# Kernel optimization log

Hardware: AMD Instinct MI355X
Metric: run time of the kernel (lower is better)

Reference implementation:

```python
import jax, jax.numpy as jnp
import numpy as np

HIDDEN = 1536
BOTTLENECK = 128
LN_EPS = 1e-5


def setup_inputs() -> dict:
    key = jax.random.key(0)
    k1, k2, k3 = jax.random.split(key, 3)
    hidden_states = jax.random.normal(k1, (4, 4096, HIDDEN), dtype=jnp.float32)
    # xavier_uniform with gain=0.01: bound = gain * sqrt(6/(fan_in+fan_out))
    bound = 0.01 * np.sqrt(6.0 / (HIDDEN + BOTTLENECK))
    w_down = jax.random.uniform(k2, (BOTTLENECK, HIDDEN), minval=-bound, maxval=bound, dtype=jnp.float32)
    w_up = jax.random.uniform(k3, (HIDDEN, BOTTLENECK), minval=-bound, maxval=bound, dtype=jnp.float32)
    ln_gamma = jnp.ones((HIDDEN,), dtype=jnp.float32)
    ln_beta = jnp.zeros((HIDDEN,), dtype=jnp.float32)
    return {"hidden_states": hidden_states, "w_down": w_down, "w_up": w_up,
            "ln_gamma": ln_gamma, "ln_beta": ln_beta}


def _fourier_2d(x):
    # fp32 FFT round-trip along seq (axis=1) then feature (axis=2), ortho norm
    orig_dtype = x.dtype
    xf = x.astype(jnp.float32)
    f = jnp.fft.fft(xf, axis=1, norm='ortho')
    f = jnp.fft.fft(f, axis=2, norm='ortho')
    t = jnp.fft.ifft(f, axis=2, norm='ortho')
    t = jnp.fft.ifft(t, axis=1, norm='ortho')
    return jnp.real(t).astype(orig_dtype)


def reference(hidden_states, w_down, w_up, ln_gamma, ln_beta):
    residual = hidden_states
    # down_proj: [b,s,H] @ [H,B] -> [b,s,B]   (nn.Linear uses x @ W^T)
    x = jnp.einsum('bsh,dh->bsd', hidden_states, w_down)
    # dropout is identity in eval mode
    x = _fourier_2d(x)
    # up_proj: [b,s,B] -> [b,s,H]
    x = jnp.einsum('bsd,hd->bsh', x, w_up)
    y = residual + x
    mu = jnp.mean(y, axis=-1, keepdims=True)
    var = jnp.mean(jnp.square(y - mu), axis=-1, keepdims=True)
    return (y - mu) * jax.lax.rsqrt(var + LN_EPS) * ln_gamma + ln_beta
```

## Files before the change

### kernel.cpp

```cpp
#include <hip/hip_runtime.h>

#define H 1536
#define BD 128
#define ROWS 16
#define NTHREADS 512
#define NBLOCKS 1024

using f16x8 = _Float16 __attribute__((ext_vector_type(8)));
using f16x4 = _Float16 __attribute__((ext_vector_type(4)));
using f32x4 = float __attribute__((ext_vector_type(4)));
using i64x2 = long __attribute__((ext_vector_type(2)));

#define WD_SCALE 16384.0f
#define T8_SCALE (1.0f/128.0f)
#define X_SCALE  (1.0f/2097152.0f)

__global__ __launch_bounds__(256) void pack_weights(const float* __restrict__ wd,
                                                    const float* __restrict__ wu,
                                                    char* __restrict__ wdp8,
                                                    char* __restrict__ wup8) {
    int f = blockIdx.x * 256 + threadIdx.x;
    const float* src;
    char* dst;
    if (f < 24576) {
        int w = f / 3072, rem = f - w * 3072;
        int ph = rem >> 6, l = rem & 63;
        int row = 16 * w + (l & 15);
        int col = 32 * ph + 8 * (l >> 4);
        src = wd + (size_t)row * H + col;
        int p = ph >> 1, half = ph & 1;
        dst = wdp8 + (((size_t)(w * 24 + p) * 64 + l) * 16 + half * 8);
    } else {
        int g = f - 24576;
        int w = g / 3072, rem = g - w * 3072;
        int t2 = rem >> 6, l = rem & 63;
        int nf = t2 >> 2, kf = t2 & 3;
        int row = 192 * w + 16 * nf + (l & 15);
        int col = 32 * kf + 8 * (l >> 4);
        src = wu + (size_t)row * BD + col;
        int q = nf * 2 + (kf >> 1), half = kf & 1;
        dst = wup8 + (((size_t)(w * 24 + q) * 64 + l) * 16 + half * 8);
    }
    float4 v0 = reinterpret_cast<const float4*>(src)[0];
    float4 v1 = reinterpret_cast<const float4*>(src)[1];
    int i0 = __builtin_amdgcn_cvt_pk_fp8_f32(v0.x * WD_SCALE, v0.y * WD_SCALE, 0, false);
    i0     = __builtin_amdgcn_cvt_pk_fp8_f32(v0.z * WD_SCALE, v0.w * WD_SCALE, i0, true);
    int i1 = __builtin_amdgcn_cvt_pk_fp8_f32(v1.x * WD_SCALE, v1.y * WD_SCALE, 0, false);
    i1     = __builtin_amdgcn_cvt_pk_fp8_f32(v1.z * WD_SCALE, v1.w * WD_SCALE, i1, true);
    int2 st = {i0, i1};
    *reinterpret_cast<int2*>(dst) = st;
}

__global__ __launch_bounds__(NTHREADS, 4) void fused_adapter(
    const float* __restrict__ hs,
    const char* __restrict__ wdp8,
    const char* __restrict__ wup8,
    const float* __restrict__ gamma,
    const float* __restrict__ beta,
    float* __restrict__ out)
{
    __shared__ alignas(16) char smem[76800];
    _Float16* hsb = reinterpret_cast<_Float16*>(smem);
    char* hsa8    = smem + 49152;
    char* tb8     = smem + 73728;
    float* redS   = reinterpret_cast<float*>(smem + 75776);
    float* redQ   = redS + 128;

    const int tid  = threadIdx.x;
    const int lane = tid & 63;
    const int w    = tid >> 6;
    const int l15  = lane & 15;
    const int lk   = lane >> 4;
    const long row0 = (long)blockIdx.x * ROWS;
    const float* hsblk = hs + row0 * H;

    const i64x2* wp2 = reinterpret_cast<const i64x2*>(wdp8) + (size_t)w * 24 * 64 + lane;
    const i64x2* up2 = reinterpret_cast<const i64x2*>(wup8) + (size_t)w * 24 * 64 + lane;

    const int sr  = tid >> 5;
    const int scg = tid & 31;
    const int swzs = (sr & 7) << 3;
    const float* srow = hsblk + (long)sr * H + scg * 8;

    auto store_chunk = [&](int c, float4 va, float4 vb) {
        int col8 = 8 * scg + 256 * c;
        f16x8 hv;
        hv[0] = (_Float16)va.x; hv[1] = (_Float16)va.y;
        hv[2] = (_Float16)va.z; hv[3] = (_Float16)va.w;
        hv[4] = (_Float16)vb.x; hv[5] = (_Float16)vb.y;
        hv[6] = (_Float16)vb.z; hv[7] = (_Float16)vb.w;
        *reinterpret_cast<f16x8*>(&hsb[sr * H + (col8 ^ swzs)]) = hv;
        int c8 = scg + 32 * c;
        int kk = c8 >> 2, m = c8 & 3;
        int al = (16 * m + sr) ^ ((kk & 15) << 1);
        int j0 = __builtin_amdgcn_cvt_pk_fp8_f32(va.x, va.y, 0, false);
        j0     = __builtin_amdgcn_cvt_pk_fp8_f32(va.z, va.w, j0, true);
        int j1 = __builtin_amdgcn_cvt_pk_fp8_f32(vb.x, vb.y, 0, false);
        j1     = __builtin_amdgcn_cvt_pk_fp8_f32(vb.z, vb.w, j1, true);
        int2 stv = {j0, j1};
        *reinterpret_cast<int2*>(&hsa8[(kk * 64 + al) * 8]) = stv;
    };

    i64x2 bq[4];
#pragma unroll
    for (int i = 0; i < 4; ++i) bq[i] = wp2[i * 64];

    float4 A0, B0, A1, B1;
    A0 = reinterpret_cast<const float4*>(srow)[0];
    B0 = reinterpret_cast<const float4*>(srow)[1];
    A1 = reinterpret_cast<const float4*>(srow + 256)[0];
    B1 = reinterpret_cast<const float4*>(srow + 256)[1];
    store_chunk(0, A0, B0);
    store_chunk(1, A1, B1);
    __syncthreads();

    f32x4 accv[4] = {{0,0,0,0},{0,0,0,0},{0,0,0,0},{0,0,0,0}};
#pragma unroll
    for (int g = 0; g < 3; ++g) {
        if (g < 2) {
            const float4* p0 = reinterpret_cast<const float4*>(srow + 256 * (2 * g + 2));
            const float4* p1 = reinterpret_cast<const float4*>(srow + 256 * (2 * g + 3));
            A0 = p0[0]; B0 = p0[1];
            A1 = p1[0]; B1 = p1[1];
        }
#pragma unroll
        for (int i = 0; i < 8; ++i) {
            int p = 8 * g + i;
            int kk0 = 2 * p, kk1 = 2 * p + 1;
            long blo = *reinterpret_cast<const long*>(&hsa8[(kk0 * 64 + (lane ^ ((kk0 & 15) << 1))) * 8]);
            long bhi = *reinterpret_cast<const long*>(&hsa8[(kk1 * 64 + (lane ^ ((kk1 & 15) << 1))) * 8]);
            i64x2 b = bq[p & 3];
            if (p + 4 < 24) bq[p & 3] = wp2[(p + 4) * 64];
            f32x4 a = accv[p & 3];
            a = __builtin_amdgcn_mfma_f32_16x16x32_fp8_fp8(b[0], blo, a, 0, 0, 0);
            a = __builtin_amdgcn_mfma_f32_16x16x32_fp8_fp8(b[1], bhi, a, 0, 0, 0);
            accv[p & 3] = a;
        }
        if (g < 2) {
            store_chunk(2 * g + 2, A0, B0);
            store_chunk(2 * g + 3, A1, B1);
            __syncthreads();
        }
    }

    i64x2 uq[4];
#pragma unroll
    for (int i = 0; i < 4; ++i) uq[i] = up2[i * 64];

    {
        f32x4 t0 = (accv[0] + accv[1]) + (accv[2] + accv[3]);
        int p0 = __builtin_amdgcn_cvt_pk_fp8_f32(t0[0] * T8_SCALE, t0[1] * T8_SCALE, 0, false);
        int p1 = __builtin_amdgcn_cvt_pk_fp8_f32(t0[2] * T8_SCALE, t0[3] * T8_SCALE, 0, false);
        unsigned word = (unsigned)(p0 & 0xFFFF) | ((unsigned)(p1 & 0xFFFF) << 16);
        int c0 = 16 * w + 4 * lk;
        int kf = c0 >> 5, hi = (c0 >> 3) & 3, off = c0 & 7;
        *reinterpret_cast<unsigned*>(&tb8[(kf * 64 + hi * 16 + l15) * 8 + off]) = word;
    }
    __syncthreads();

    long a2f8[4];
#pragma unroll
    for (int kf = 0; kf < 4; ++kf)
        a2f8[kf] = *reinterpret_cast<const long*>(&tb8[(kf * 64 + lane) * 8]);

    float s = 0.f, q = 0.f;
#pragma unroll
    for (int nf = 0; nf < 12; ++nf) {
        i64x2 u0 = uq[(2 * nf) & 3];
        i64x2 u1 = uq[(2 * nf + 1) & 3];
        if (2 * nf + 4 < 24) uq[(2 * nf) & 3]     = up2[(2 * nf + 4) * 64];
        if (2 * nf + 5 < 24) uq[(2 * nf + 1) & 3] = up2[(2 * nf + 5) * 64];
        f32x4 acc = {0.f, 0.f, 0.f, 0.f};
        acc = __builtin_amdgcn_mfma_f32_16x16x32_fp8_fp8(u0[0], a2f8[0], acc, 0, 0, 0);
        acc = __builtin_amdgcn_mfma_f32_16x16x32_fp8_fp8(u0[1], a2f8[1], acc, 0, 0, 0);
        acc = __builtin_amdgcn_mfma_f32_16x16x32_fp8_fp8(u1[0], a2f8[2], acc, 0, 0, 0);
        acc = __builtin_amdgcn_mfma_f32_16x16x32_fp8_fp8(u1[1], a2f8[3], acc, 0, 0, 0);
        int cx = 192 * w + 16 * nf + 4 * lk;
        int idx = l15 * H + (cx ^ ((l15 & 7) << 3));
        f16x4 hv4 = *reinterpret_cast<const f16x4*>(&hsb[idx]);
        float y0 = acc[0] * X_SCALE + (float)hv4[0];
        float y1 = acc[1] * X_SCALE + (float)hv4[1];
        float y2 = acc[2] * X_SCALE + (float)hv4[2];
        float y3 = acc[3] * X_SCALE + (float)hv4[3];
        s += (y0 + y1) + (y2 + y3);
        q += (y0 * y0 + y1 * y1) + (y2 * y2 + y3 * y3);
        f16x4 yv;
        yv[0] = (_Float16)y0; yv[1] = (_Float16)y1;
        yv[2] = (_Float16)y2; yv[3] = (_Float16)y3;
        *reinterpret_cast<f16x4*>(&hsb[idx]) = yv;
    }

    s += __shfl_xor(s, 16); s += __shfl_xor(s, 32);
    q += __shfl_xor(q, 16); q += __shfl_xor(q, 32);
    if (lane < 16) {
        redS[w * 16 + lane] = s;
        redQ[w * 16 + lane] = q;
    }
    __syncthreads();

    {
        const int fr  = tid >> 5;
        const int cid = tid & 31;
        const int fswz = (fr & 7) << 3;
        float S = 0.f, Q = 0.f;
#pragma unroll
        for (int ww = 0; ww < 8; ++ww) {
            S += redS[ww * 16 + fr];
            Q += redQ[ww * 16 + fr];
        }
        float mean = S * (1.0f / (float)H);
        float var  = Q * (1.0f / (float)H) - mean * mean;
        float rstd = rsqrtf(var + 1e-5f);
        float* orow = out + (row0 + fr) * H;
#pragma unroll
        for (int k = 0; k < 6; ++k) {
            int col = 8 * (cid + 32 * k);
            f16x8 yv = *reinterpret_cast<const f16x8*>(&hsb[fr * H + (col ^ fswz)]);
            const float4* gp = reinterpret_cast<const float4*>(gamma + col);
            const float4* bp = reinterpret_cast<const float4*>(beta + col);
            float4 g0 = gp[0], g1 = gp[1];
            float4 b0 = bp[0], b1 = bp[1];
            float4 o0, o1;
            o0.x = ((float)yv[0] - mean) * rstd * g0.x + b0.x;
            o0.y = ((float)yv[1] - mean) * rstd * g0.y + b0.y;
            o0.z = ((float)yv[2] - mean) * rstd * g0.z + b0.z;
            o0.w = ((float)yv[3] - mean) * rstd * g0.w + b0.w;
            o1.x = ((float)yv[4] - mean) * rstd * g1.x + b1.x;
            o1.y = ((float)yv[5] - mean) * rstd * g1.y + b1.y;
            o1.z = ((float)yv[6] - mean) * rstd * g1.z + b1.z;
            o1.w = ((float)yv[7] - mean) * rstd * g1.w + b1.w;
            float4* op = reinterpret_cast<float4*>(orow + col);
            op[0] = o0;
            op[1] = o1;
        }
    }
}

extern "C" void kernel_launch(void* const* d_in, const int* in_sizes, int n_in,
                              void* d_out, int out_size, void* d_ws, size_t ws_size,
                              hipStream_t stream) {
    const float* hs    = (const float*)d_in[0];
    const float* wd    = (const float*)d_in[1];
    const float* wu    = (const float*)d_in[2];
    const float* gam   = (const float*)d_in[3];
    const float* bet   = (const float*)d_in[4];
    float* out = (float*)d_out;

    char* wdp8 = (char*)d_ws;
    char* wup8 = (char*)d_ws + (size_t)128 * H;

    pack_weights<<<192, 256, 0, stream>>>(wd, wu, wdp8, wup8);
    fused_adapter<<<NBLOCKS, NTHREADS, 0, stream>>>(hs, wdp8, wup8, gam, bet, out);
}
```

Before: 56.25 us.

## Make blocks process four row tiles with double-buffered LDS prefetch

Each block now handles four 16-row tiles instead of one, and the grid shrinks to 256 blocks. The LDS staging buffers are double-buffered so the next tile's hidden states are loaded, converted and stored in chunks interleaved with the current tile's down-projection, up-projection and LayerNorm phases. The aim is to hide global-load latency behind compute and to avoid the per-block prologue. In exchange, LDS use roughly doubles to about 150 KB per block, which allows only one block per CU. Each thread also keeps only one chunk of loads in flight, so memory-level parallelism may drop.

```diff
diff --git a/kernel.cpp b/kernel.cpp
--- a/kernel.cpp
+++ b/kernel.cpp
@@ -4,7 +4,7 @@
 #define BD 128
 #define ROWS 16
 #define NTHREADS 512
-#define NBLOCKS 1024
+#define NBLOCKS 256
 
 using f16x8 = _Float16 __attribute__((ext_vector_type(8)));
 using f16x4 = _Float16 __attribute__((ext_vector_type(4)));
@@ -51,7 +51,7 @@
     *reinterpret_cast<int2*>(dst) = st;
 }
 
-__global__ __launch_bounds__(NTHREADS, 4) void fused_adapter(
+__global__ __launch_bounds__(NTHREADS, 2) void fused_adapter(
     const float* __restrict__ hs,
     const char* __restrict__ wdp8,
     const char* __restrict__ wup8,
@@ -59,20 +59,21 @@
     const float* __restrict__ beta,
     float* __restrict__ out)
 {
-    __shared__ alignas(16) char smem[76800];
-    _Float16* hsb = reinterpret_cast<_Float16*>(smem);
-    char* hsa8    = smem + 49152;
-    char* tb8     = smem + 73728;
-    float* redS   = reinterpret_cast<float*>(smem + 75776);
-    float* redQ   = redS + 128;
+    __shared__ alignas(16) char smem[150528];
+    _Float16* hsbP = reinterpret_cast<_Float16*>(smem);
+    char*     hsa8P = smem + 49152;
+    _Float16* hsbQ = reinterpret_cast<_Float16*>(smem + 73728);
+    char*     hsa8Q = smem + 122880;
+    char*     tb8   = smem + 147456;
+    float*    redS  = reinterpret_cast<float*>(smem + 149504);
+    float*    redQ  = redS + 128;
 
     const int tid  = threadIdx.x;
     const int lane = tid & 63;
     const int w    = tid >> 6;
     const int l15  = lane & 15;
     const int lk   = lane >> 4;
-    const long row0 = (long)blockIdx.x * ROWS;
-    const float* hsblk = hs + row0 * H;
+    const long row0 = (long)blockIdx.x * (4 * ROWS);
 
     const i64x2* wp2 = reinterpret_cast<const i64x2*>(wdp8) + (size_t)w * 24 * 64 + lane;
     const i64x2* up2 = reinterpret_cast<const i64x2*>(wup8) + (size_t)w * 24 * 64 + lane;
@@ -80,16 +81,15 @@
     const int sr  = tid >> 5;
     const int scg = tid & 31;
     const int swzs = (sr & 7) << 3;
-    const float* srow = hsblk + (long)sr * H + scg * 8;
-
-    auto store_chunk = [&](int c, float4 va, float4 vb) {
+
+    auto store_chunk = [&](_Float16* hsb_, char* hsa8_, int c, float4 va, float4 vb) {
         int col8 = 8 * scg + 256 * c;
         f16x8 hv;
         hv[0] = (_Float16)va.x; hv[1] = (_Float16)va.y;
         hv[2] = (_Float16)va.z; hv[3] = (_Float16)va.w;
         hv[4] = (_Float16)vb.x; hv[5] = (_Float16)vb.y;
         hv[6] = (_Float16)vb.z; hv[7] = (_Float16)vb.w;
-        *reinterpret_cast<f16x8*>(&hsb[sr * H + (col8 ^ swzs)]) = hv;
+        *reinterpret_cast<f16x8*>(&hsb_[sr * H + (col8 ^ swzs)]) = hv;
         int c8 = scg + 32 * c;
         int kk = c8 >> 2, m = c8 & 3;
         int al = (16 * m + sr) ^ ((kk & 15) << 1);
@@ -98,141 +98,173 @@
         int j1 = __builtin_amdgcn_cvt_pk_fp8_f32(vb.x, vb.y, 0, false);
         j1     = __builtin_amdgcn_cvt_pk_fp8_f32(vb.z, vb.w, j1, true);
         int2 stv = {j0, j1};
-        *reinterpret_cast<int2*>(&hsa8[(kk * 64 + al) * 8]) = stv;
+        *reinterpret_cast<int2*>(&hsa8_[(kk * 64 + al) * 8]) = stv;
     };
 
-    i64x2 bq[4];
-#pragma unroll
-    for (int i = 0; i < 4; ++i) bq[i] = wp2[i * 64];
-
-    float4 A0, B0, A1, B1;
-    A0 = reinterpret_cast<const float4*>(srow)[0];
-    B0 = reinterpret_cast<const float4*>(srow)[1];
-    A1 = reinterpret_cast<const float4*>(srow + 256)[0];
-    B1 = reinterpret_cast<const float4*>(srow + 256)[1];
-    store_chunk(0, A0, B0);
-    store_chunk(1, A1, B1);
-    __syncthreads();
-
-    f32x4 accv[4] = {{0,0,0,0},{0,0,0,0},{0,0,0,0},{0,0,0,0}};
-#pragma unroll
-    for (int g = 0; g < 3; ++g) {
-        if (g < 2) {
-            const float4* p0 = reinterpret_cast<const float4*>(srow + 256 * (2 * g + 2));
-            const float4* p1 = reinterpret_cast<const float4*>(srow + 256 * (2 * g + 3));
-            A0 = p0[0]; B0 = p0[1];
-            A1 = p1[0]; B1 = p1[1];
-        }
-#pragma unroll
-        for (int i = 0; i < 8; ++i) {
-            int p = 8 * g + i;
-            int kk0 = 2 * p, kk1 = 2 * p + 1;
-            long blo = *reinterpret_cast<const long*>(&hsa8[(kk0 * 64 + (lane ^ ((kk0 & 15) << 1))) * 8]);
-            long bhi = *reinterpret_cast<const long*>(&hsa8[(kk1 * 64 + (lane ^ ((kk1 & 15) << 1))) * 8]);
-            i64x2 b = bq[p & 3];
-            if (p + 4 < 24) bq[p & 3] = wp2[(p + 4) * 64];
-            f32x4 a = accv[p & 3];
-            a = __builtin_amdgcn_mfma_f32_16x16x32_fp8_fp8(b[0], blo, a, 0, 0, 0);
-            a = __builtin_amdgcn_mfma_f32_16x16x32_fp8_fp8(b[1], bhi, a, 0, 0, 0);
-            accv[p & 3] = a;
-        }
-        if (g < 2) {
-            store_chunk(2 * g + 2, A0, B0);
-            store_chunk(2 * g + 3, A1, B1);
-            __syncthreads();
-        }
-    }
-
-    i64x2 uq[4];
-#pragma unroll
-    for (int i = 0; i < 4; ++i) uq[i] = up2[i * 64];
-
     {
-        f32x4 t0 = (accv[0] + accv[1]) + (accv[2] + accv[3]);
-        int p0 = __builtin_amdgcn_cvt_pk_fp8_f32(t0[0] * T8_SCALE, t0[1] * T8_SCALE, 0, false);
-        int p1 = __builtin_amdgcn_cvt_pk_fp8_f32(t0[2] * T8_SCALE, t0[3] * T8_SCALE, 0, false);
-        unsigned word = (unsigned)(p0 & 0xFFFF) | ((unsigned)(p1 & 0xFFFF) << 16);
-        int c0 = 16 * w + 4 * lk;
-        int kf = c0 >> 5, hi = (c0 >> 3) & 3, off = c0 & 7;
-        *reinterpret_cast<unsigned*>(&tb8[(kf * 64 + hi * 16 + l15) * 8 + off]) = word;
+        const float* srow0 = hs + (row0 + sr) * H + scg * 8;
+#pragma unroll
+        for (int pp = 0; pp < 3; ++pp) {
+            const float4* p0 = reinterpret_cast<const float4*>(srow0 + 256 * (2 * pp));
+            const float4* p1 = reinterpret_cast<const float4*>(srow0 + 256 * (2 * pp + 1));
+            float4 a0 = p0[0], b0 = p0[1];
+            float4 a1 = p1[0], b1 = p1[1];
+            store_chunk(hsbP, hsa8P, 2 * pp, a0, b0);
+            store_chunk(hsbP, hsa8P, 2 * pp + 1, a1, b1);
+        }
     }
     __syncthreads();
 
-    long a2f8[4];
-#pragma unroll
-    for (int kf = 0; kf < 4; ++kf)
-        a2f8[kf] = *reinterpret_cast<const long*>(&tb8[(kf * 64 + lane) * 8]);
-
-    float s = 0.f, q = 0.f;
-#pragma unroll
-    for (int nf = 0; nf < 12; ++nf) {
-        i64x2 u0 = uq[(2 * nf) & 3];
-        i64x2 u1 = uq[(2 * nf + 1) & 3];
-        if (2 * nf + 4 < 24) uq[(2 * nf) & 3]     = up2[(2 * nf + 4) * 64];
-        if (2 * nf + 5 < 24) uq[(2 * nf + 1) & 3] = up2[(2 * nf + 5) * 64];
-        f32x4 acc = {0.f, 0.f, 0.f, 0.f};
-        acc = __builtin_amdgcn_mfma_f32_16x16x32_fp8_fp8(u0[0], a2f8[0], acc, 0, 0, 0);
-        acc = __builtin_amdgcn_mfma_f32_16x16x32_fp8_fp8(u0[1], a2f8[1], acc, 0, 0, 0);
-        acc = __builtin_amdgcn_mfma_f32_16x16x32_fp8_fp8(u1[0], a2f8[2], acc, 0, 0, 0);
-        acc = __builtin_amdgcn_mfma_f32_16x16x32_fp8_fp8(u1[1], a2f8[3], acc, 0, 0, 0);
-        int cx = 192 * w + 16 * nf + 4 * lk;
-        int idx = l15 * H + (cx ^ ((l15 & 7) << 3));
-        f16x4 hv4 = *reinterpret_cast<const f16x4*>(&hsb[idx]);
-        float y0 = acc[0] * X_SCALE + (float)hv4[0];
-        float y1 = acc[1] * X_SCALE + (float)hv4[1];
-        float y2 = acc[2] * X_SCALE + (float)hv4[2];
-        float y3 = acc[3] * X_SCALE + (float)hv4[3];
-        s += (y0 + y1) + (y2 + y3);
-        q += (y0 * y0 + y1 * y1) + (y2 * y2 + y3 * y3);
-        f16x4 yv;
-        yv[0] = (_Float16)y0; yv[1] = (_Float16)y1;
-        yv[2] = (_Float16)y2; yv[3] = (_Float16)y3;
-        *reinterpret_cast<f16x4*>(&hsb[idx]) = yv;
-    }
-
-    s += __shfl_xor(s, 16); s += __shfl_xor(s, 32);
-    q += __shfl_xor(q, 16); q += __shfl_xor(q, 32);
-    if (lane < 16) {
-        redS[w * 16 + lane] = s;
-        redQ[w * 16 + lane] = q;
-    }
-    __syncthreads();
-
-    {
-        const int fr  = tid >> 5;
-        const int cid = tid & 31;
-        const int fswz = (fr & 7) << 3;
-        float S = 0.f, Q = 0.f;
-#pragma unroll
-        for (int ww = 0; ww < 8; ++ww) {
-            S += redS[ww * 16 + fr];
-            Q += redQ[ww * 16 + fr];
-        }
-        float mean = S * (1.0f / (float)H);
-        float var  = Q * (1.0f / (float)H) - mean * mean;
-        float rstd = rsqrtf(var + 1e-5f);
-        float* orow = out + (row0 + fr) * H;
-#pragma unroll
-        for (int k = 0; k < 6; ++k) {
-            int col = 8 * (cid + 32 * k);
-            f16x8 yv = *reinterpret_cast<const f16x8*>(&hsb[fr * H + (col ^ fswz)]);
-            const float4* gp = reinterpret_cast<const float4*>(gamma + col);
-            const float4* bp = reinterpret_cast<const float4*>(beta + col);
-            float4 g0 = gp[0], g1 = gp[1];
-            float4 b0 = bp[0], b1 = bp[1];
-            float4 o0, o1;
-            o0.x = ((float)yv[0] - mean) * rstd * g0.x + b0.x;
-            o0.y = ((float)yv[1] - mean) * rstd * g0.y + b0.y;
-            o0.z = ((float)yv[2] - mean) * rstd * g0.z + b0.z;
-            o0.w = ((float)yv[3] - mean) * rstd * g0.w + b0.w;
-            o1.x = ((float)yv[4] - mean) * rstd * g1.x + b1.x;
-            o1.y = ((float)yv[5] - mean) * rstd * g1.y + b1.y;
-            o1.z = ((float)yv[6] - mean) * rstd * g1.z + b1.z;
-            o1.w = ((float)yv[7] - mean) * rstd * g1.w + b1.w;
-            float4* op = reinterpret_cast<float4*>(orow + col);
-            op[0] = o0;
-            op[1] = o1;
-        }
+#pragma unroll
+    for (int t = 0; t < 4; ++t) {
+        _Float16* chsb  = (t & 1) ? hsbQ : hsbP;
+        char*     chsa8 = (t & 1) ? hsa8Q : hsa8P;
+        _Float16* nhsb  = (t & 1) ? hsbP : hsbQ;
+        char*     nhsa8 = (t & 1) ? hsa8P : hsa8Q;
+        const bool stg = (t < 3);
+        const float* hsblk = hs + (row0 + (long)t * ROWS) * H;
+        float* outblk = out + (row0 + (long)t * ROWS) * H;
+        const float* nsrow = stg ? hs + (row0 + (long)(t + 1) * ROWS + sr) * H + scg * 8
+                                 : hsblk;
+
+        float4 fA, fB;
+        if (stg) {
+            const float4* p = reinterpret_cast<const float4*>(nsrow);
+            fA = p[0]; fB = p[1];
+        }
+
+        i64x2 bq[4];
+#pragma unroll
+        for (int i = 0; i < 4; ++i) bq[i] = wp2[i * 64];
+
+        f32x4 accv[4] = {{0,0,0,0},{0,0,0,0},{0,0,0,0},{0,0,0,0}};
+#pragma unroll
+        for (int g = 0; g < 3; ++g) {
+#pragma unroll
+            for (int i = 0; i < 8; ++i) {
+                int p = 8 * g + i;
+                int kk0 = 2 * p, kk1 = 2 * p + 1;
+                long blo = *reinterpret_cast<const long*>(&chsa8[(kk0 * 64 + (lane ^ ((kk0 & 15) << 1))) * 8]);
+                long bhi = *reinterpret_cast<const long*>(&chsa8[(kk1 * 64 + (lane ^ ((kk1 & 15) << 1))) * 8]);
+                i64x2 b = bq[p & 3];
+                if (p + 4 < 24) bq[p & 3] = wp2[(p + 4) * 64];
+                f32x4 a = accv[p & 3];
+                a = __builtin_amdgcn_mfma_f32_16x16x32_fp8_fp8(b[0], blo, a, 0, 0, 0);
+                a = __builtin_amdgcn_mfma_f32_16x16x32_fp8_fp8(b[1], bhi, a, 0, 0, 0);
+                accv[p & 3] = a;
+            }
+            if (stg) {
+                store_chunk(nhsb, nhsa8, g, fA, fB);
+                const float4* p = reinterpret_cast<const float4*>(nsrow + 256 * (g + 1));
+                fA = p[0]; fB = p[1];
+            }
+        }
+
+        i64x2 uq[4];
+#pragma unroll
+        for (int i = 0; i < 4; ++i) uq[i] = up2[i * 64];
+
+        {
+            f32x4 t0 = (accv[0] + accv[1]) + (accv[2] + accv[3]);
+            int p0 = __builtin_amdgcn_cvt_pk_fp8_f32(t0[0] * T8_SCALE, t0[1] * T8_SCALE, 0, false);
+            int p1 = __builtin_amdgcn_cvt_pk_fp8_f32(t0[2] * T8_SCALE, t0[3] * T8_SCALE, 0, false);
+            unsigned word = (unsigned)(p0 & 0xFFFF) | ((unsigned)(p1 & 0xFFFF) << 16);
+            int c0 = 16 * w + 4 * lk;
+            int kf = c0 >> 5, hi = (c0 >> 3) & 3, off = c0 & 7;
+            *reinterpret_cast<unsigned*>(&tb8[(kf * 64 + hi * 16 + l15) * 8 + off]) = word;
+        }
+        __syncthreads();
+
+        long a2f8[4];
+#pragma unroll
+        for (int kf = 0; kf < 4; ++kf)
+            a2f8[kf] = *reinterpret_cast<const long*>(&tb8[(kf * 64 + lane) * 8]);
+
+        float s = 0.f, q = 0.f;
+#pragma unroll
+        for (int nf = 0; nf < 12; ++nf) {
+            i64x2 u0 = uq[(2 * nf) & 3];
+            i64x2 u1 = uq[(2 * nf + 1) & 3];
+            if (2 * nf + 4 < 24) uq[(2 * nf) & 3]     = up2[(2 * nf + 4) * 64];
+            if (2 * nf + 5 < 24) uq[(2 * nf + 1) & 3] = up2[(2 * nf + 5) * 64];
+            f32x4 acc = {0.f, 0.f, 0.f, 0.f};
+            acc = __builtin_amdgcn_mfma_f32_16x16x32_fp8_fp8(u0[0], a2f8[0], acc, 0, 0, 0);
+            acc = __builtin_amdgcn_mfma_f32_16x16x32_fp8_fp8(u0[1], a2f8[1], acc, 0, 0, 0);
+            acc = __builtin_amdgcn_mfma_f32_16x16x32_fp8_fp8(u1[0], a2f8[2], acc, 0, 0, 0);
+            acc = __builtin_amdgcn_mfma_f32_16x16x32_fp8_fp8(u1[1], a2f8[3], acc, 0, 0, 0);
+            int cx = 192 * w + 16 * nf + 4 * lk;
+            int idx = l15 * H + (cx ^ ((l15 & 7) << 3));
+            f16x4 hv4 = *reinterpret_cast<const f16x4*>(&chsb[idx]);
+            float y0 = acc[0] * X_SCALE + (float)hv4[0];
+            float y1 = acc[1] * X_SCALE + (float)hv4[1];
+            float y2 = acc[2] * X_SCALE + (float)hv4[2];
+            float y3 = acc[3] * X_SCALE + (float)hv4[3];
+            s += (y0 + y1) + (y2 + y3);
+            q += (y0 * y0 + y1 * y1) + (y2 * y2 + y3 * y3);
+            f16x4 yv;
+            yv[0] = (_Float16)y0; yv[1] = (_Float16)y1;
+            yv[2] = (_Float16)y2; yv[3] = (_Float16)y3;
+            *reinterpret_cast<f16x4*>(&chsb[idx]) = yv;
+            if (stg && nf == 5) {
+                store_chunk(nhsb, nhsa8, 3, fA, fB);
+                const float4* p = reinterpret_cast<const float4*>(nsrow + 256 * 4);
+                fA = p[0]; fB = p[1];
+            }
+            if (stg && nf == 11) {
+                store_chunk(nhsb, nhsa8, 4, fA, fB);
+                const float4* p = reinterpret_cast<const float4*>(nsrow + 256 * 5);
+                fA = p[0]; fB = p[1];
+            }
+        }
+
+        s += __shfl_xor(s, 16); s += __shfl_xor(s, 32);
+        q += __shfl_xor(q, 16); q += __shfl_xor(q, 32);
+        if (lane < 16) {
+            redS[w * 16 + lane] = s;
+            redQ[w * 16 + lane] = q;
+        }
+        __syncthreads();
+
+        {
+            const int fr  = tid >> 5;
+            const int cid = tid & 31;
+            const int fswz = (fr & 7) << 3;
+            float S = 0.f, Q = 0.f;
+#pragma unroll
+            for (int ww = 0; ww < 8; ++ww) {
+                S += redS[ww * 16 + fr];
+                Q += redQ[ww * 16 + fr];
+            }
+            float mean = S * (1.0f / (float)H);
+            float var  = Q * (1.0f / (float)H) - mean * mean;
+            float rstd = rsqrtf(var + 1e-5f);
+            float* orow = outblk + (long)fr * H;
+#pragma unroll
+            for (int k = 0; k < 6; ++k) {
+                int col = 8 * (cid + 32 * k);
+                f16x8 yv = *reinterpret_cast<const f16x8*>(&chsb[fr * H + (col ^ fswz)]);
+                const float4* gp = reinterpret_cast<const float4*>(gamma + col);
+                const float4* bp = reinterpret_cast<const float4*>(beta + col);
+                float4 g0 = gp[0], g1 = gp[1];
+                float4 b0 = bp[0], b1 = bp[1];
+                float4 o0, o1;
+                o0.x = ((float)yv[0] - mean) * rstd * g0.x + b0.x;
+                o0.y = ((float)yv[1] - mean) * rstd * g0.y + b0.y;
+                o0.z = ((float)yv[2] - mean) * rstd * g0.z + b0.z;
+                o0.w = ((float)yv[3] - mean) * rstd * g0.w + b0.w;
+                o1.x = ((float)yv[4] - mean) * rstd * g1.x + b1.x;
+                o1.y = ((float)yv[5] - mean) * rstd * g1.y + b1.y;
+                o1.z = ((float)yv[6] - mean) * rstd * g1.z + b1.z;
+                o1.w = ((float)yv[7] - mean) * rstd * g1.w + b1.w;
+                float4* op = reinterpret_cast<float4*>(orow + col);
+                op[0] = o0;
+                op[1] = o1;
+                if (stg && k == 2) {
+                    store_chunk(nhsb, nhsa8, 5, fA, fB);
+                }
+            }
+        }
+        __syncthreads();
     }
 }
 
```

Result: slower. 70.64 us (+25.6%).
